# Kernel optimization log

Measured on AMD Instinct MI355X. Metric: run time of the kernel, lower is better.

Reference implementation:

```python
import jax, jax.numpy as jnp
import numpy as np
import math

HORIZONS = (1, 5, 21)
TEMP = 0.07
N_NEG = 128
B, T, D = 16, 512, 256


def _normalize(x):
    # F.normalize(dim=-1): x / max(||x||, eps)
    return x / jnp.maximum(jnp.linalg.norm(x, axis=-1, keepdims=True), 1e-12)


def setup_inputs() -> dict:
    key = jax.random.key(0)
    k1, k2, k3 = jax.random.split(key, 3)
    z_seq = jax.random.normal(k1, (B, T, D), dtype=jnp.float32)
    # stacked per-horizon Linear weights (nn.Linear applies x @ W.T)
    preds = jax.random.normal(k2, (len(HORIZONS), D, D), dtype=jnp.float32) / np.float32(np.sqrt(D))
    neg_idx = jax.random.randint(k3, (len(HORIZONS), B * T, N_NEG), 0, B * T, dtype=jnp.int64)
    return {"z_seq": z_seq, "preds": preds, "neg_idx": neg_idx}


def reference(z_seq, preds, neg_idx):
    raw_w = {k: 1.0 / math.sqrt(k) for k in HORIZONS}
    tot_w = sum(raw_w.values())
    # detached, normalized pool of all timesteps used as negatives
    all_z = jax.lax.stop_gradient(_normalize(z_seq.reshape(B * T, D)))
    total = jnp.float32(0.0)
    for i, k in enumerate(HORIZONS):
        if k >= T:
            continue
        L = T - k
        # predictor: Linear without bias -> anchor @ W.T
        z_pred = jnp.einsum('bld,ed->ble', z_seq[:, :L, :], preds[i]).reshape(B * L, D)
        z_pred = _normalize(z_pred)
        z_pos = jax.lax.stop_gradient(_normalize(z_seq[:, k:, :].reshape(B * L, D)))
        idx = neg_idx[i, :B * L]                    # [B*L, N_NEG]
        z_neg = all_z[idx]                          # [B*L, N_NEG, D]
        pos_logit = jnp.sum(z_pred * z_pos, axis=-1, keepdims=True) / TEMP   # [B*L, 1]
        neg_logits = jnp.einsum('nkd,nd->nk', z_neg, z_pred) / TEMP          # [B*L, N_NEG]
        logits = jnp.concatenate([pos_logit, neg_logits], axis=1)
        # cross-entropy with label 0
        loss = jnp.mean(jax.nn.logsumexp(logits, axis=1) - logits[:, 0])
        total = total + jnp.float32(raw_w[k] / tot_w) * loss
    return total
```

## Files before the change

kernel.cpp:

```cpp
#include <hip/hip_runtime.h>
#include <math.h>

constexpr int Bc = 16, Tc = 512, Dc = 256, NNEGc = 128, BTc = Bc * Tc;
constexpr float TEMP_INV = 1.0f / 0.07f;
constexpr float SCALE4 = 21.875f;
constexpr float QSCALE4 = TEMP_INV / (SCALE4 * SCALE4);
constexpr float FMAXL = TEMP_INV;
constexpr int GX = 2043;
constexpr int NPART = 3 * GX;

typedef __attribute__((ext_vector_type(8))) short short8;
typedef __attribute__((ext_vector_type(4))) float f32x4;
typedef __attribute__((ext_vector_type(4))) _Float16 f16x4;
typedef __attribute__((ext_vector_type(2))) _Float16 h2;

struct HP { int L, N, kh; float scale; long long nxOff; };
struct HP3 { HP h[3]; };

__device__ inline unsigned packh2(float a, float b) {
    h2 p = {(_Float16)a, (_Float16)b};
    return __builtin_bit_cast(unsigned, p);
}
__device__ inline float dot2(unsigned a, unsigned b, float c) {
#if __has_builtin(__builtin_amdgcn_fdot2)
    return __builtin_amdgcn_fdot2(__builtin_bit_cast(h2, a), __builtin_bit_cast(h2, b), c, false);
#else
    h2 x = __builtin_bit_cast(h2, a), y = __builtin_bit_cast(h2, b);
    return c + (float)x.x * (float)y.x + (float)x.y * (float)y.y;
#endif
}
__device__ inline int sdot8(unsigned a, unsigned b, int c) {
#if __has_builtin(__builtin_amdgcn_sdot8)
    return __builtin_amdgcn_sdot8((int)a, (int)b, c, false);
#else
#pragma unroll
    for (int i = 0; i < 8; ++i) {
        int xa = ((int)(a << (28 - 4 * i))) >> 28;
        int xb = ((int)(b << (28 - 4 * i))) >> 28;
        c += xa * xb;
    }
    return c;
#endif
}
__device__ inline unsigned q4x4(float a, float b, float c, float d) {
    int qa = (int)rintf(fminf(fmaxf(a * SCALE4, -7.0f), 7.0f));
    int qb = (int)rintf(fminf(fmaxf(b * SCALE4, -7.0f), 7.0f));
    int qc = (int)rintf(fminf(fmaxf(c * SCALE4, -7.0f), 7.0f));
    int qd = (int)rintf(fminf(fmaxf(d * SCALE4, -7.0f), 7.0f));
    return (qa & 0xF) | ((qb & 0xF) << 4) | ((qc & 0xF) << 8) | ((qd & 0xF) << 12);
}

__global__ __launch_bounds__(256) void k_norm(const float* __restrict__ z,
                                              const float* __restrict__ preds,
                                              unsigned* __restrict__ az,
                                              unsigned short* __restrict__ ani4,
                                              unsigned* __restrict__ Wh) {
    if (blockIdx.x < 96) {
        int base = blockIdx.x * 2048 + threadIdx.x * 8;
        float4 w0 = reinterpret_cast<const float4*>(preds + base)[0];
        float4 w1 = reinterpret_cast<const float4*>(preds + base)[1];
        uint4 o;
        o.x = packh2(w0.x, w0.y); o.y = packh2(w0.z, w0.w);
        o.z = packh2(w1.x, w1.y); o.w = packh2(w1.z, w1.w);
        reinterpret_cast<uint4*>(Wh)[blockIdx.x * 256 + threadIdx.x] = o;
    }
    int wid = threadIdx.x >> 6, lane = threadIdx.x & 63;
    int row = blockIdx.x * 4 + wid;
    float4 v = reinterpret_cast<const float4*>(z)[row * 64 + lane];
    float s = v.x * v.x + v.y * v.y + v.z * v.z + v.w * v.w;
#pragma unroll
    for (int off = 32; off; off >>= 1) s += __shfl_xor(s, off, 64);
    float inv = 1.0f / fmaxf(sqrtf(s), 1e-12f);
    float a = v.x * inv, b = v.y * inv, c = v.z * inv, d = v.w * inv;
    reinterpret_cast<uint2*>(az)[row * 64 + lane] = make_uint2(packh2(a, b), packh2(c, d));
    ani4[row * 64 + lane] = (unsigned short)q4x4(a, b, c, d);
}

__global__ __launch_bounds__(256) void k_gemm(const unsigned* __restrict__ az,
                                              const unsigned* __restrict__ Wh,
                                              _Float16* __restrict__ zp) {
    __shared__ uint4 As[2048];
    __shared__ uint4 Bs[2048];
    int wave = threadIdx.x >> 6, lane = threadIdx.x & 63;
    int t = threadIdx.x;
    int m0 = blockIdx.x * 64, g0 = blockIdx.y * 64;
    const uint4* A4 = reinterpret_cast<const uint4*>(az) + (size_t)m0 * 32;
    const uint4* B4 = reinterpret_cast<const uint4*>(Wh) + (size_t)g0 * 32;
#pragma unroll
    for (int i = 0; i < 8; ++i) {
        int f = i * 256 + t;
        int r = f >> 5, c = f & 31;
        int sw = r * 32 + ((c ^ r) & 31);
        As[sw] = A4[f];
        Bs[sw] = B4[f];
    }
    __syncthreads();
    int mrow = lane & 15, kq = lane >> 4;
    f32x4 acc[4] = {f32x4{0,0,0,0}, f32x4{0,0,0,0}, f32x4{0,0,0,0}, f32x4{0,0,0,0}};
    int arow = wave * 16 + mrow;
#pragma unroll
    for (int kb = 0; kb < 8; ++kb) {
        int col = kb * 4 + kq;
        uint4 ua = As[arow * 32 + ((col ^ arow) & 31)];
        short8 a = __builtin_bit_cast(short8, ua);
#pragma unroll
        for (int nt = 0; nt < 4; ++nt) {
            int brow = nt * 16 + mrow;
            uint4 ub = Bs[brow * 32 + ((col ^ brow) & 31)];
            acc[nt] = __builtin_amdgcn_mfma_f32_16x16x32_f16(
                a, __builtin_bit_cast(short8, ub), acc[nt], 0, 0, 0);
        }
    }
#pragma unroll
    for (int nt = 0; nt < 4; ++nt) {
        int g = g0 + nt * 16 + mrow;
        int h = g >> 8, e = g & 255;
        _Float16* dst = zp + ((size_t)h * BTc + m0 + wave * 16 + kq * 4) * Dc + e;
#pragma unroll
        for (int r = 0; r < 4; ++r) dst[(size_t)r * Dc] = (_Float16)acc[nt][r];
    }
}

__global__ __launch_bounds__(256, 4) void k_loss(const unsigned* __restrict__ az,
                                                 const unsigned* __restrict__ ani4,
                                                 const _Float16* __restrict__ zp_base,
                                                 const int* __restrict__ nx_base,
                                                 float* __restrict__ partials,
                                                 HP3 P) {
    HP hp = P.h[blockIdx.y];
    __shared__ uint4 zqm[4][8];
    __shared__ float partial[4];
    int wid = threadIdx.x >> 6, lane = threadIdx.x & 63;
    int g = lane >> 3, s = lane & 7;
    int n = blockIdx.x * 4 + wid;
    float contrib = 0.0f;
    if (n < hp.N) {
        const int* nx = nx_base + hp.nxOff + (size_t)n * NNEGc;
        int i1 = nx[lane], i2 = nx[lane + 64];
        const uint4* ni4 = reinterpret_cast<const uint4*>(ani4);
        int ia = __shfl(i1, 0 * 8 + g, 64);
        int ib = __shfl(i1, 1 * 8 + g, 64);
        uint4 buf[2][2];
        buf[0][0] = ni4[(size_t)ia * 8 + s];
        buf[0][1] = ni4[(size_t)ib * 8 + s];

        int b = n / hp.L, l = n - b * hp.L;
        int row = b * Tc + l;
        f16x4 hv = reinterpret_cast<const f16x4*>(
                       zp_base + ((size_t)blockIdx.y * BTc + row) * Dc)[lane];
        uint2 pw = reinterpret_cast<const uint2*>(az + (size_t)(row + hp.kh) * 128)[lane];
        float4 v = make_float4((float)hv.x, (float)hv.y, (float)hv.z, (float)hv.w);
        float sq = v.x * v.x + v.y * v.y + v.z * v.z + v.w * v.w;
#pragma unroll
        for (int off = 32; off; off >>= 1) sq += __shfl_xor(sq, off, 64);
        float inv = 1.0f / fmaxf(sqrtf(sq), 1e-12f);
        v.x *= inv; v.y *= inv; v.z *= inv; v.w *= inv;
        reinterpret_cast<unsigned short*>(zqm[wid])[lane] =
            (unsigned short)q4x4(v.x, v.y, v.z, v.w);
        float pd = dot2(pw.y, packh2(v.z, v.w), dot2(pw.x, packh2(v.x, v.y), 0.0f));
#pragma unroll
        for (int off = 32; off; off >>= 1) pd += __shfl_xor(pd, off, 64);
        float pos = pd * TEMP_INV;
        uint4 zs = zqm[wid][s];

        float sl = 0.0f;
#pragma unroll
        for (int k = 0; k < 8; ++k) {
            int cur = k & 1, nxt = cur ^ 1;
            if (k < 7) {
                int p0 = 2 * k + 2, p1 = 2 * k + 3;
                int na = __shfl(p0 < 8 ? i1 : i2, (p0 & 7) * 8 + g, 64);
                int nb = __shfl(p1 < 8 ? i1 : i2, (p1 & 7) * 8 + g, 64);
                buf[nxt][0] = ni4[(size_t)na * 8 + s];
                buf[nxt][1] = ni4[(size_t)nb * 8 + s];
            }
            uint4 ga = buf[cur][0], gb = buf[cur][1];
            int aa = 0, ab = 0;
            aa = sdot8(ga.x, zs.x, aa); aa = sdot8(ga.y, zs.y, aa);
            aa = sdot8(ga.z, zs.z, aa); aa = sdot8(ga.w, zs.w, aa);
            ab = sdot8(gb.x, zs.x, ab); ab = sdot8(gb.y, zs.y, ab);
            ab = sdot8(gb.z, zs.z, ab); ab = sdot8(gb.w, zs.w, ab);
            unsigned pk = ((unsigned)(aa + 2048) << 16) | (unsigned)(ab + 2048);
            pk += (unsigned)__shfl_xor((int)pk, 1, 64);
            pk += (unsigned)__shfl_xor((int)pk, 2, 64);
            pk += (unsigned)__shfl_xor((int)pk, 4, 64);
            float la = (float)((int)(pk >> 16) - 16384);
            float lb = (float)((int)(pk & 0xffffu) - 16384);
            sl += __expf(la * QSCALE4 - FMAXL) + __expf(lb * QSCALE4 - FMAXL);
        }
        sl += __shfl_xor(sl, 8, 64);
        sl += __shfl_xor(sl, 16, 64);
        sl += __shfl_xor(sl, 32, 64);
        float S = sl + __expf(pos - FMAXL);
        contrib = (FMAXL + __logf(S) - pos) * hp.scale;
    }
    if (lane == 0) partial[wid] = contrib;
    __syncthreads();
    if (threadIdx.x == 0)
        partials[blockIdx.y * GX + blockIdx.x] =
            partial[0] + partial[1] + partial[2] + partial[3];
}

__global__ __launch_bounds__(256) void k_final(const float* __restrict__ partials,
                                               float* __restrict__ out) {
    __shared__ float ws[4];
    int wid = threadIdx.x >> 6, lane = threadIdx.x & 63;
    float s = 0.0f;
    for (int i = threadIdx.x; i < NPART; i += 256) s += partials[i];
#pragma unroll
    for (int off = 32; off; off >>= 1) s += __shfl_xor(s, off, 64);
    if (lane == 0) ws[wid] = s;
    __syncthreads();
    if (threadIdx.x == 0) out[0] = ws[0] + ws[1] + ws[2] + ws[3];
}

extern "C" void kernel_launch(void* const* d_in, const int* in_sizes, int n_in,
                              void* d_out, int out_size, void* d_ws, size_t ws_size,
                              hipStream_t stream) {
    const float* z     = (const float*)d_in[0];
    const float* preds = (const float*)d_in[1];
    const int*   nidx  = (const int*)d_in[2];
    float* out = (float*)d_out;

    unsigned*       az   = (unsigned*)d_ws;
    unsigned short* ani4 = (unsigned short*)((char*)d_ws + (size_t)4194304);
    unsigned*       Wh   = (unsigned*)((char*)d_ws + (size_t)5242880);
    _Float16*       zp   = (_Float16*)((char*)d_ws + (size_t)5636096);
    float*          part = (float*)((char*)d_ws + (size_t)18219008);

    const int ks[3] = {1, 5, 21};
    double rw[3] = {1.0, 1.0 / sqrt(5.0), 1.0 / sqrt(21.0)};
    double tot = rw[0] + rw[1] + rw[2];

    HP3 P;
    for (int i = 0; i < 3; ++i) {
        int L = Tc - ks[i], N = Bc * L;
        P.h[i].L = L; P.h[i].N = N; P.h[i].kh = ks[i];
        P.h[i].scale = (float)(rw[i] / tot / (double)N);
        P.h[i].nxOff = (long long)i * BTc * NNEGc;
    }

    k_norm<<<BTc / 4, 256, 0, stream>>>(z, preds, az, ani4, Wh);
    k_gemm<<<dim3(BTc / 64, (3 * Dc) / 64), 256, 0, stream>>>(az, Wh, zp);
    k_loss<<<dim3(GX, 3), 256, 0, stream>>>(az, (const unsigned*)ani4, zp, nidx, part, P);
    k_final<<<1, 256, 0, stream>>>(part, out);
}
```

Baseline: 105.4 us.

## Regroup negative gather to 4 lanes per row with DPP reductions

Each negative row is now handled by 4 lanes, each loading two 16-byte chunks, instead of 8 lanes loading one chunk each. Negative indices are loaded directly into a lane layout that DPP quad-broadcast can read, which replaces ds_bpermute shuffles. The gather is restructured into 4 fully prefetched stages with deeper lookahead. The intra-quad reductions also use DPP instead of shuffles. This trades higher register use, which may lower occupancy, for fewer shuffle instructions and more memory-level parallelism in the gather.

Measured after the change: 104.3 us. About the same (-1.0%).

```diff
diff --git a/kernel.cpp b/kernel.cpp
--- a/kernel.cpp
+++ b/kernel.cpp
@@ -16,6 +16,10 @@
 
 struct HP { int L, N, kh; float scale; long long nxOff; };
 struct HP3 { HP h[3]; };
+
+#define DPP_I(x, ctrl) __builtin_amdgcn_update_dpp(0, (x), (ctrl), 0xF, 0xF, true)
+#define FDPP_XOR1(x) __builtin_bit_cast(float, DPP_I(__builtin_bit_cast(int, (x)), 0xB1))
+#define FDPP_XOR2(x) __builtin_bit_cast(float, DPP_I(__builtin_bit_cast(int, (x)), 0x4E))
 
 __device__ inline unsigned packh2(float a, float b) {
     h2 p = {(_Float16)a, (_Float16)b};
@@ -131,18 +135,26 @@
     __shared__ uint4 zqm[4][8];
     __shared__ float partial[4];
     int wid = threadIdx.x >> 6, lane = threadIdx.x & 63;
-    int g = lane >> 3, s = lane & 7;
+    int g = lane >> 2, s = lane & 3;
     int n = blockIdx.x * 4 + wid;
     float contrib = 0.0f;
     if (n < hp.N) {
         const int* nx = nx_base + hp.nxOff + (size_t)n * NNEGc;
-        int i1 = nx[lane], i2 = nx[lane + 64];
+        int ja = nx[32 * s + g];
+        int jb = nx[32 * s + 16 + g];
         const uint4* ni4 = reinterpret_cast<const uint4*>(ani4);
-        int ia = __shfl(i1, 0 * 8 + g, 64);
-        int ib = __shfl(i1, 1 * 8 + g, 64);
-        uint4 buf[2][2];
-        buf[0][0] = ni4[(size_t)ia * 8 + s];
-        buf[0][1] = ni4[(size_t)ib * 8 + s];
+
+        uint4 bA0[4], bA1[4], bB0[4], bB1[4];
+#define CPC_PREF(K, CTRL)                                                     \
+        {                                                                     \
+            int ia_ = DPP_I(ja, CTRL), ib_ = DPP_I(jb, CTRL);                 \
+            bA0[K] = ni4[(size_t)ia_ * 8 + s];                                \
+            bA1[K] = ni4[(size_t)ia_ * 8 + 4 + s];                            \
+            bB0[K] = ni4[(size_t)ib_ * 8 + s];                                \
+            bB1[K] = ni4[(size_t)ib_ * 8 + 4 + s];                            \
+        }
+        CPC_PREF(0, 0x00)
+        CPC_PREF(1, 0x55)
 
         int b = n / hp.L, l = n - b * hp.L;
         int row = b * Tc + l;
@@ -151,46 +163,59 @@
         uint2 pw = reinterpret_cast<const uint2*>(az + (size_t)(row + hp.kh) * 128)[lane];
         float4 v = make_float4((float)hv.x, (float)hv.y, (float)hv.z, (float)hv.w);
         float sq = v.x * v.x + v.y * v.y + v.z * v.z + v.w * v.w;
-#pragma unroll
-        for (int off = 32; off; off >>= 1) sq += __shfl_xor(sq, off, 64);
+        sq += FDPP_XOR1(sq);
+        sq += FDPP_XOR2(sq);
+        sq += __shfl_xor(sq, 4, 64);
+        sq += __shfl_xor(sq, 8, 64);
+        sq += __shfl_xor(sq, 16, 64);
+        sq += __shfl_xor(sq, 32, 64);
         float inv = 1.0f / fmaxf(sqrtf(sq), 1e-12f);
         v.x *= inv; v.y *= inv; v.z *= inv; v.w *= inv;
         reinterpret_cast<unsigned short*>(zqm[wid])[lane] =
             (unsigned short)q4x4(v.x, v.y, v.z, v.w);
         float pd = dot2(pw.y, packh2(v.z, v.w), dot2(pw.x, packh2(v.x, v.y), 0.0f));
-#pragma unroll
-        for (int off = 32; off; off >>= 1) pd += __shfl_xor(pd, off, 64);
-        float pos = pd * TEMP_INV;
-        uint4 zs = zqm[wid][s];
+        uint4 zsa = zqm[wid][s];
+        uint4 zsb = zqm[wid][4 + s];
 
         float sl = 0.0f;
-#pragma unroll
-        for (int k = 0; k < 8; ++k) {
-            int cur = k & 1, nxt = cur ^ 1;
-            if (k < 7) {
-                int p0 = 2 * k + 2, p1 = 2 * k + 3;
-                int na = __shfl(p0 < 8 ? i1 : i2, (p0 & 7) * 8 + g, 64);
-                int nb = __shfl(p1 < 8 ? i1 : i2, (p1 & 7) * 8 + g, 64);
-                buf[nxt][0] = ni4[(size_t)na * 8 + s];
-                buf[nxt][1] = ni4[(size_t)nb * 8 + s];
-            }
-            uint4 ga = buf[cur][0], gb = buf[cur][1];
-            int aa = 0, ab = 0;
-            aa = sdot8(ga.x, zs.x, aa); aa = sdot8(ga.y, zs.y, aa);
-            aa = sdot8(ga.z, zs.z, aa); aa = sdot8(ga.w, zs.w, aa);
-            ab = sdot8(gb.x, zs.x, ab); ab = sdot8(gb.y, zs.y, ab);
-            ab = sdot8(gb.z, zs.z, ab); ab = sdot8(gb.w, zs.w, ab);
-            unsigned pk = ((unsigned)(aa + 2048) << 16) | (unsigned)(ab + 2048);
-            pk += (unsigned)__shfl_xor((int)pk, 1, 64);
-            pk += (unsigned)__shfl_xor((int)pk, 2, 64);
-            pk += (unsigned)__shfl_xor((int)pk, 4, 64);
-            float la = (float)((int)(pk >> 16) - 16384);
-            float lb = (float)((int)(pk & 0xffffu) - 16384);
-            sl += __expf(la * QSCALE4 - FMAXL) + __expf(lb * QSCALE4 - FMAXL);
+#define CPC_COMP(K)                                                           \
+        {                                                                     \
+            int aa = 0, ab = 0;                                               \
+            aa = sdot8(bA0[K].x, zsa.x, aa); aa = sdot8(bA0[K].y, zsa.y, aa); \
+            aa = sdot8(bA0[K].z, zsa.z, aa); aa = sdot8(bA0[K].w, zsa.w, aa); \
+            aa = sdot8(bA1[K].x, zsb.x, aa); aa = sdot8(bA1[K].y, zsb.y, aa); \
+            aa = sdot8(bA1[K].z, zsb.z, aa); aa = sdot8(bA1[K].w, zsb.w, aa); \
+            ab = sdot8(bB0[K].x, zsa.x, ab); ab = sdot8(bB0[K].y, zsa.y, ab); \
+            ab = sdot8(bB0[K].z, zsa.z, ab); ab = sdot8(bB0[K].w, zsa.w, ab); \
+            ab = sdot8(bB1[K].x, zsb.x, ab); ab = sdot8(bB1[K].y, zsb.y, ab); \
+            ab = sdot8(bB1[K].z, zsb.z, ab); ab = sdot8(bB1[K].w, zsb.w, ab); \
+            unsigned pk = ((unsigned)(aa + 4096) << 16) | (unsigned)(ab + 4096); \
+            pk += (unsigned)DPP_I((int)pk, 0xB1);                             \
+            pk += (unsigned)DPP_I((int)pk, 0x4E);                             \
+            float la = (float)((int)(pk >> 16) - 16384);                      \
+            float lb = (float)((int)(pk & 0xffffu) - 16384);                  \
+            sl += __expf(la * QSCALE4 - FMAXL) + __expf(lb * QSCALE4 - FMAXL); \
         }
+        CPC_PREF(2, 0xAA)
+        CPC_COMP(0)
+        CPC_PREF(3, 0xFF)
+        CPC_COMP(1)
+        CPC_COMP(2)
+        CPC_COMP(3)
+#undef CPC_PREF
+#undef CPC_COMP
+
+        sl += __shfl_xor(sl, 4, 64);
         sl += __shfl_xor(sl, 8, 64);
         sl += __shfl_xor(sl, 16, 64);
         sl += __shfl_xor(sl, 32, 64);
+        pd += FDPP_XOR1(pd);
+        pd += FDPP_XOR2(pd);
+        pd += __shfl_xor(pd, 4, 64);
+        pd += __shfl_xor(pd, 8, 64);
+        pd += __shfl_xor(pd, 16, 64);
+        pd += __shfl_xor(pd, 32, 64);
+        float pos = pd * TEMP_INV;
         float S = sl + __expf(pos - FMAXL);
         contrib = (FMAXL + __logf(S) - pos) * hp.scale;
     }
```
